# Performance work log

Hardware: AMD Instinct MI355X
Metric: run time of the kernel (lower is better)

Reference implementation:

```python
import jax, jax.numpy as jnp
import numpy as np

SEGMENT_LENGTHS = [2048, 4096, 8192]
DILATION_RATES = [1, 2, 4]
RING_SIZE = 4


def _head_groups(h, g):
    base, rem = divmod(h, g)
    return [base + (1 if i < rem else 0) for i in range(g)]


def _dilation_pattern(n, seg, r, group_idx):
    # Per-segment dilated index pattern of total length n (index_select target).
    s = min(seg, n)
    off = group_idx % r
    base = (off + np.arange(0, s, r)) % s          # stride-r indices within segment
    pat_seg = np.tile(base, r)[:s]                  # repeat to fill segment length
    nseg = n // s
    pat = (pat_seg[None, :] + np.arange(nseg)[:, None] * s).reshape(-1)
    return pat


def _apply_dilation(x):
    # x: (b, n, h, d). Gather along sequence per head group.
    b, n, h, d = x.shape
    groups = _head_groups(h, len(SEGMENT_LENGTHS))
    outs, hs = [], 0
    for i, (seg, r, g) in enumerate(zip(SEGMENT_LENGTHS, DILATION_RATES, groups)):
        if g == 0:
            continue
        pat = jnp.asarray(_dilation_pattern(n, seg, r, i))
        outs.append(x[:, pat, hs:hs + g, :])
        hs += g
    return jnp.concatenate(outs, axis=2)


def setup_inputs() -> dict:
    key = jax.random.key(0)
    k1, k2, k3 = jax.random.split(key, 3)
    shape = (1, 8192, 16, 64)
    return {
        "q": jax.random.normal(k1, shape, dtype=jnp.float32),
        "k": jax.random.normal(k2, shape, dtype=jnp.float32),
        "v": jax.random.normal(k3, shape, dtype=jnp.float32),
    }


def reference(q, k, v):
    b, n, h, d = q.shape
    scale = 1.0 / jnp.sqrt(jnp.asarray(d, q.dtype))
    chunk = n // RING_SIZE

    # Dilate queries once; dilate each local KV chunk (ring-distributed layout).
    qt = _apply_dilation(q).transpose(0, 2, 1, 3)   # (b, h, n, d)

    acc_out = jnp.zeros((b, h, n, d), q.dtype)
    acc_lse = jnp.full((b, h, n), -jnp.inf, q.dtype)

    # Simulated ring pass: iterate over KV chunks with online-LSE accumulation.
    for c in range(RING_SIZE):
        kc = _apply_dilation(k[:, c * chunk:(c + 1) * chunk])  # (b, chunk, h, d)
        vc = _apply_dilation(v[:, c * chunk:(c + 1) * chunk])
        scores = jnp.einsum('bhqd,bkhd->bhqk', qt, kc) * scale
        lse_c = jax.nn.logsumexp(scores, axis=-1)              # (b, h, n)
        out_c = jnp.einsum('bhqk,bkhd->bhqd',
                           jax.nn.softmax(scores, axis=-1), vc)
        new_lse = jnp.logaddexp(acc_lse, lse_c)
        w_old = jnp.exp(acc_lse - new_lse)[..., None]
        w_new = jnp.exp(lse_c - new_lse)[..., None]
        acc_out = w_old * acc_out + w_new * out_c
        acc_lse = new_lse

    return acc_out.transpose(0, 2, 1, 3)  # (b, n, h, d)
```

## Files before the change

kernel.cpp:

```cpp
#include <hip/hip_runtime.h>
#include <hip/hip_bf16.h>
#include <math.h>

typedef __attribute__((ext_vector_type(4))) float f32x4;
typedef __attribute__((ext_vector_type(8))) short bf16x8;
typedef __attribute__((ext_vector_type(4))) short s16x4;

#define NH 16
#define HD 64
#define BM 128
#define BM2 256
#define BN 64
#define WM 32
#define LDS_K 72
#define TILE2_B 16384
#define WS_FB 0ull

#define OPART5_OFF 20447232ull
#define LPART5_OFF (OPART5_OFF + 25165824ull)
#define WS5_NEEDED (LPART5_OFF + 393216ull)

__device__ __forceinline__ short f2bf(float f) {
    union { float f; unsigned u; } x; x.f = f;
    unsigned r = x.u + 0x7fffu + ((x.u >> 16) & 1u);
    return (short)(r >> 16);
}
__device__ __forceinline__ unsigned pack2bf(float a, float b) {
    union { float f; unsigned u; } x, y; x.f = a; y.f = b;
    return __builtin_amdgcn_perm(y.u + 0x8000u, x.u + 0x8000u, 0x07060302u);
}
__device__ __forceinline__ float elem(const float4& r, int j) {
    return ((const float*)&r)[j];
}
__device__ __forceinline__ size_t head_base2(int h) {
    if (h < 6)  return (size_t)h * (128 * TILE2_B);
    if (h < 11) return 6ull * (128 * TILE2_B) + (size_t)(h - 6) * (64 * TILE2_B);
    return 6ull * (128 * TILE2_B) + 5ull * (64 * TILE2_B) + (size_t)(h - 11) * (32 * TILE2_B);
}

__global__ __launch_bounds__(256)
void rda_pack2(const float* __restrict__ K, const float* __restrict__ V, char* __restrict__ W) {
    int bid = blockIdx.x;
    int h, t, type;
    if (bid < 768)       { type = 0; h = bid >> 7;                t = bid & 127; }
    else if (bid < 1088) { type = 1; h = 6 + ((bid - 768) >> 6);  t = (bid - 768) & 63; }
    else                 { type = 2; h = 11 + ((bid - 1088) >> 5); t = (bid - 1088) & 31; }
    int rate = 1 << type, off = type;
    char* tile = W + head_base2(h) + (size_t)t * TILE2_B;
    int tid = threadIdx.x;
    {
        int row = tid >> 2, c = (tid & 3) * 16;
        int pos = rate * (t * 64 + row) + off;
        const float* p = K + ((size_t)pos * NH + h) * HD + c;
        float4 a0 = ((const float4*)p)[0], a1 = ((const float4*)p)[1];
        float4 a2 = ((const float4*)p)[2], a3 = ((const float4*)p)[3];
        uint4 d0, d1;
        d0.x = pack2bf(elem(a0,0), elem(a0,1)); d0.y = pack2bf(elem(a0,2), elem(a0,3));
        d0.z = pack2bf(elem(a1,0), elem(a1,1)); d0.w = pack2bf(elem(a1,2), elem(a1,3));
        d1.x = pack2bf(elem(a2,0), elem(a2,1)); d1.y = pack2bf(elem(a2,2), elem(a2,3));
        d1.z = pack2bf(elem(a3,0), elem(a3,1)); d1.w = pack2bf(elem(a3,2), elem(a3,3));
        int L = row * 128 + c * 2;
        int sw = (row & 7) << 4;
        *(uint4*)(tile + (L ^ sw)) = d0;
        *(uint4*)(tile + ((L + 16) ^ sw)) = d1;
    }
    {
        int vr = (tid & 15) * 4, vc = (tid >> 4) * 4;
        float4 vv[4];
#pragma unroll
        for (int i = 0; i < 4; ++i) {
            int pos = rate * (t * 64 + vr + i) + off;
            vv[i] = *(const float4*)(V + ((size_t)pos * NH + h) * HD + vc);
        }
#pragma unroll
        for (int j = 0; j < 4; ++j) {
            uint2 w;
            w.x = pack2bf(elem(vv[0], j), elem(vv[1], j));
            w.y = pack2bf(elem(vv[2], j), elem(vv[3], j));
            int rr = vc + j;
            int L = rr * 128 + vr * 2;
            *(uint2*)(tile + 8192 + (L ^ ((rr & 7) << 4))) = w;
        }
    }
}

__global__ __launch_bounds__(512, 4)
void rda_attn_w8s(const float* __restrict__ Q, char* __restrict__ W, float* __restrict__ O) {
    __shared__ __align__(16) short sKV[2 * 8192];
    __shared__ __align__(16) short sP[8][1024];

    int bid = blockIdx.x;
    int h, mb, type, kc, nst, sid;
    if (bid < 384)      { type = 0; h = bid >> 6; int rem = bid & 63; mb = rem >> 1; kc = rem & 1; nst = 64; sid = bid; }
    else if (bid < 464) { type = 1; int rel = bid - 384; h = 6 + (rel >> 4); mb = rel & 15; kc = 0; nst = 64; sid = -1; }
    else                { type = 2; int rel = bid - 464; h = 11 + (rel >> 3); mb = rel & 7; kc = 0; nst = 32; sid = -1; }
    int rate = 1 << type;
    int off  = type;
    int kb0  = kc * 64;

    int tid  = threadIdx.x;
    int wave = tid >> 6;
    int lane = tid & 63;
    int ln   = lane & 15;
    int quad = lane >> 4;

    const float SC = 0.125f * 1.4426950408889634f;

    int qbase = mb * BM2 + wave * WM;
    bf16x8 qf[2][2];
#pragma unroll
    for (int mt = 0; mt < 2; ++mt) {
        int u = qbase + mt * 16 + ln;
        size_t base = ((size_t)(rate * u + off) * NH + h) * HD;
#pragma unroll
        for (int ks = 0; ks < 2; ++ks) {
            const float* p = Q + base + ks * 32 + quad * 8;
            float4 a = ((const float4*)p)[0];
            float4 b = ((const float4*)p)[1];
            union { uint4 u4; bf16x8 f; } cv;
            cv.u4.x = pack2bf(elem(a,0)*SC, elem(a,1)*SC);
            cv.u4.y = pack2bf(elem(a,2)*SC, elem(a,3)*SC);
            cv.u4.z = pack2bf(elem(b,0)*SC, elem(b,1)*SC);
            cv.u4.w = pack2bf(elem(b,2)*SC, elem(b,3)*SC);
            qf[mt][ks] = cv.f;
        }
    }

    f32x4 acc[2][4];
#pragma unroll
    for (int mt = 0; mt < 2; ++mt)
#pragma unroll
        for (int dt = 0; dt < 4; ++dt) acc[mt][dt] = (f32x4){0.f, 0.f, 0.f, 0.f};
    float lp[2] = {0.f, 0.f};

    const char* gh = W + head_base2(h);

    auto stage = [&](const char* gt, int lB) {
#pragma unroll
        for (int r = 0; r < 2; ++r) {
            int c = r * 8192 + tid * 16;
            __builtin_amdgcn_global_load_lds(
                (const __attribute__((address_space(1))) unsigned*)(gt + c),
                (__attribute__((address_space(3))) unsigned*)((char*)sKV + lB + c),
                16, 0, 0);
        }
    };

    stage(gh + (size_t)kb0 * TILE2_B, 0);
    int pB = 0;

    char* pbase = (char*)&sP[wave][0];

    for (int i = 0; i < nst; ++i) {
        int kb = kb0 + i;
        __syncthreads();

        if (i + 1 < nst) stage(gh + (size_t)(kb + 1) * TILE2_B, pB ^ TILE2_B);

        const char* sKb = (const char*)sKV + pB;
        const char* sVb = sKb + 8192;

#pragma unroll
        for (int x = 0; x < 2; ++x) {
            f32x4 st[2][2];
            __builtin_amdgcn_s_setprio(1);
#pragma unroll
            for (int kk = 0; kk < 2; ++kk) {
                int ra = (2 * x + kk) * 16 + ln;
                int sw = (ra & 7) << 4;
                bf16x8 a0 = *(const bf16x8*)(sKb + ((ra * 128 + quad * 16) ^ sw));
                bf16x8 a1 = *(const bf16x8*)(sKb + ((ra * 128 + 64 + quad * 16) ^ sw));
#pragma unroll
                for (int mt = 0; mt < 2; ++mt) {
                    f32x4 c = (f32x4){0.f, 0.f, 0.f, 0.f};
                    c = __builtin_amdgcn_mfma_f32_16x16x32_bf16(a0, qf[mt][0], c, 0, 0, 0);
                    c = __builtin_amdgcn_mfma_f32_16x16x32_bf16(a1, qf[mt][1], c, 0, 0, 0);
                    st[kk][mt] = c;
                }
            }
            __builtin_amdgcn_s_setprio(0);

#pragma unroll
            for (int mt = 0; mt < 2; ++mt)
#pragma unroll
                for (int kk = 0; kk < 2; ++kk) {
                    float p0 = __builtin_amdgcn_exp2f(st[kk][mt][0]);
                    float p1 = __builtin_amdgcn_exp2f(st[kk][mt][1]);
                    float p2 = __builtin_amdgcn_exp2f(st[kk][mt][2]);
                    float p3 = __builtin_amdgcn_exp2f(st[kk][mt][3]);
                    lp[mt] += (p0 + p1) + (p2 + p3);
                    uint2 pk;
                    pk.x = pack2bf(p0, p1);
                    pk.y = pack2bf(p2, p3);
                    int prow = mt * 16 + ln;
                    int Lb = prow * 64 + kk * 32 + quad * 8;
                    *(uint2*)(pbase + (Lb ^ (((prow >> 1) & 3) << 4))) = pk;
                }
            __asm__ volatile("s_waitcnt lgkmcnt(0)" ::: "memory");

            __builtin_amdgcn_s_setprio(1);
            int b0 = (ln * 64 + quad * 16) ^ (((ln >> 1) & 3) << 4);
            int b1 = ((16 + ln) * 64 + quad * 16) ^ ((((16 + ln) >> 1) & 3) << 4);
            bf16x8 pa0 = *(bf16x8*)(pbase + b0);
            bf16x8 pa1 = *(bf16x8*)(pbase + b1);
#pragma unroll
            for (int dt = 0; dt < 4; ++dt) {
                int rv = dt * 16 + ln;
                bf16x8 vb = *(const bf16x8*)(sVb + ((rv * 128 + x * 64 + quad * 16) ^ ((rv & 7) << 4)));
                acc[0][dt] = __builtin_amdgcn_mfma_f32_16x16x32_bf16(pa0, vb, acc[0][dt], 0, 0, 0);
                acc[1][dt] = __builtin_amdgcn_mfma_f32_16x16x32_bf16(pa1, vb, acc[1][dt], 0, 0, 0);
            }
            __builtin_amdgcn_s_setprio(0);
        }
        pB ^= TILE2_B;
    }

#pragma unroll
    for (int mt = 0; mt < 2; ++mt) {
        lp[mt] += __shfl_xor(lp[mt], 16);
        lp[mt] += __shfl_xor(lp[mt], 32);
    }

    if (type == 0) {
        float* Op = (float*)(W + OPART5_OFF) + (size_t)sid * (BM2 * HD);
        float* Lp = (float*)(W + LPART5_OFF) + (size_t)sid * BM2;
#pragma unroll
        for (int mt = 0; mt < 2; ++mt) {
            if (quad == 0) Lp[wave * WM + mt * 16 + ln] = lp[mt];
#pragma unroll
            for (int r = 0; r < 4; ++r) {
                int ql = wave * WM + mt * 16 + quad * 4 + r;
#pragma unroll
                for (int dt = 0; dt < 4; ++dt)
                    Op[ql * HD + dt * 16 + ln] = acc[mt][dt][r];
            }
        }
    } else {
#pragma unroll
        for (int mt = 0; mt < 2; ++mt)
#pragma unroll
            for (int r = 0; r < 4; ++r) {
                float lO = __shfl(lp[mt], quad * 4 + r);
                float inv = 1.0f / lO;
                int u = qbase + mt * 16 + quad * 4 + r;
#pragma unroll
                for (int dt = 0; dt < 4; ++dt) {
                    float val = acc[mt][dt][r] * inv;
                    int dcol = dt * 16 + ln;
                    if (type == 1) {
                        int r0 = ((u >> 11) << 12) + (u & 2047);
                        O[((size_t)r0 * NH + h) * HD + dcol] = val;
                        O[((size_t)(r0 + 2048) * NH + h) * HD + dcol] = val;
                    } else {
#pragma unroll
                        for (int t = 0; t < 4; ++t)
                            O[((size_t)(u + t * 2048) * NH + h) * HD + dcol] = val;
                    }
                }
            }
    }
}

__global__ __launch_bounds__(256)
void rda_comb5(const char* __restrict__ W, float* __restrict__ O) {
    int c = blockIdx.x;
    int h = c >> 5, mb = c & 31;
    int s0 = c * 2;

    const float* P0 = (const float*)(W + OPART5_OFF) + (size_t)s0 * (BM2 * HD);
    const float* L0 = (const float*)(W + LPART5_OFF) + (size_t)s0 * BM2;

    __shared__ float sInv[BM2];
    int tid = threadIdx.x;
    sInv[tid] = 1.0f / (L0[tid] + L0[BM2 + tid]);
    __syncthreads();

#pragma unroll
    for (int i = 0; i < 16; ++i) {
        int f = i * 256 + tid;
        int q = f >> 4, d4 = f & 15;
        float4 a = ((const float4*)P0)[f];
        float4 b = ((const float4*)(P0 + BM2 * HD))[f];
        float inv = sInv[q];
        float4 v;
        v.x = (a.x + b.x) * inv; v.y = (a.y + b.y) * inv;
        v.z = (a.z + b.z) * inv; v.w = (a.w + b.w) * inv;
        int u = mb * BM2 + q;
        *(float4*)&O[((size_t)u * NH + h) * HD + d4 * 4] = v;
    }
}

__global__ __launch_bounds__(256, 2)
void rda_attn_fb(const float* __restrict__ Q, const float* __restrict__ K,
                 const float* __restrict__ V, float* __restrict__ O) {
    __shared__ short sK[BN * LDS_K];
    __shared__ short sVT[HD * LDS_K];
    __shared__ short sP[4][WM * LDS_K];

    int bid = blockIdx.x;
    int h, mb, type;
    if (bid < 384)      { type = 0; h = bid >> 6;               mb = bid & 63; }
    else if (bid < 544) { type = 1; h = 6 + ((bid - 384) >> 5); mb = (bid - 384) & 31; }
    else                { type = 2; h = 11 + ((bid - 544) >> 4); mb = (bid - 544) & 15; }
    int rate = 1 << type;
    int off  = type;
    int nsteps = 128 >> type;

    int tid  = threadIdx.x;
    int wave = tid >> 6;
    int lane = tid & 63;
    int ln   = lane & 15;
    int quad = lane >> 4;

    const float SC = 0.125f * 1.4426950408889634f;

    int qbase = mb * BM + wave * WM;
    bf16x8 qf[2][2];
#pragma unroll
    for (int mt = 0; mt < 2; ++mt) {
        int u = qbase + mt * 16 + ln;
        size_t base = ((size_t)(rate * u + off) * NH + h) * HD;
#pragma unroll
        for (int ks = 0; ks < 2; ++ks) {
            const float* p = Q + base + ks * 32 + quad * 8;
            float4 a = ((const float4*)p)[0];
            float4 b = ((const float4*)p)[1];
            bf16x8 f;
#pragma unroll
            for (int i = 0; i < 4; ++i) { f[i] = f2bf(elem(a, i) * SC); f[4 + i] = f2bf(elem(b, i) * SC); }
            qf[mt][ks] = f;
        }
    }

    f32x4 acc[2][4];
#pragma unroll
    for (int mt = 0; mt < 2; ++mt)
#pragma unroll
        for (int dt = 0; dt < 4; ++dt) acc[mt][dt] = (f32x4){0.f, 0.f, 0.f, 0.f};
    float m_i[2] = {-INFINITY, -INFINITY};
    float l_i[2] = {0.f, 0.f};

    int srow = tid >> 2, sc0 = (tid & 3) * 16;
    int vr = (tid >> 4) * 4, vc = (tid & 15) * 4;

    for (int kb = 0; kb < nsteps; ++kb) {
        {
            int kpos = rate * (kb * BN + srow) + off;
            const float* p = K + ((size_t)kpos * NH + h) * HD + sc0;
            float4 kv0 = ((const float4*)p)[0], kv1 = ((const float4*)p)[1];
            float4 kv2 = ((const float4*)p)[2], kv3 = ((const float4*)p)[3];
            bf16x8 f0, f1;
#pragma unroll
            for (int i = 0; i < 4; ++i) {
                f0[i] = f2bf(elem(kv0, i)); f0[4 + i] = f2bf(elem(kv1, i));
                f1[i] = f2bf(elem(kv2, i)); f1[4 + i] = f2bf(elem(kv3, i));
            }
            *(bf16x8*)&sK[srow * LDS_K + sc0] = f0;
            *(bf16x8*)&sK[srow * LDS_K + sc0 + 8] = f1;
        }
        {
            float4 vv[4];
#pragma unroll
            for (int i = 0; i < 4; ++i) {
                int kpos = rate * (kb * BN + vr + i) + off;
                vv[i] = *(const float4*)(V + ((size_t)kpos * NH + h) * HD + vc);
            }
#pragma unroll
            for (int j = 0; j < 4; ++j) {
                s16x4 t;
                t[0] = f2bf(elem(vv[0], j)); t[1] = f2bf(elem(vv[1], j));
                t[2] = f2bf(elem(vv[2], j)); t[3] = f2bf(elem(vv[3], j));
                *(s16x4*)&sVT[(vc + j) * LDS_K + vr] = t;
            }
        }
        __syncthreads();

        f32x4 st[4][2];
#pragma unroll
        for (int kt = 0; kt < 4; ++kt) {
            bf16x8 a0 = *(bf16x8*)&sK[(kt * 16 + ln) * LDS_K + quad * 8];
            bf16x8 a1 = *(bf16x8*)&sK[(kt * 16 + ln) * LDS_K + 32 + quad * 8];
#pragma unroll
            for (int mt = 0; mt < 2; ++mt) {
                f32x4 c = (f32x4){0.f, 0.f, 0.f, 0.f};
                c = __builtin_amdgcn_mfma_f32_16x16x32_bf16(a0, qf[mt][0], c, 0, 0, 0);
                c = __builtin_amdgcn_mfma_f32_16x16x32_bf16(a1, qf[mt][1], c, 0, 0, 0);
                st[kt][mt] = c;
            }
        }

#pragma unroll
        for (int mt = 0; mt < 2; ++mt) {
            float tmax = -INFINITY;
#pragma unroll
            for (int kt = 0; kt < 4; ++kt)
#pragma unroll
                for (int r = 0; r < 4; ++r) tmax = fmaxf(tmax, st[kt][mt][r]);
            tmax = fmaxf(tmax, __shfl_xor(tmax, 16));
            tmax = fmaxf(tmax, __shfl_xor(tmax, 32));
            float mnew = fmaxf(m_i[mt], tmax);
            float al = exp2f(m_i[mt] - mnew);
            m_i[mt] = mnew;
            float rs = 0.f;
#pragma unroll
            for (int kt = 0; kt < 4; ++kt)
#pragma unroll
                for (int r = 0; r < 4; ++r) {
                    float pe = exp2f(st[kt][mt][r] - mnew);
                    st[kt][mt][r] = pe;
                    rs += pe;
                }
            rs += __shfl_xor(rs, 16);
            rs += __shfl_xor(rs, 32);
            l_i[mt] = l_i[mt] * al + rs;
#pragma unroll
            for (int r = 0; r < 4; ++r) {
                float aO = __shfl(al, quad * 4 + r);
#pragma unroll
                for (int dt = 0; dt < 4; ++dt) acc[mt][dt][r] *= aO;
            }
        }

#pragma unroll
        for (int mt = 0; mt < 2; ++mt)
#pragma unroll
            for (int kt = 0; kt < 4; ++kt) {
                s16x4 pk;
                pk[0] = f2bf(st[kt][mt][0]); pk[1] = f2bf(st[kt][mt][1]);
                pk[2] = f2bf(st[kt][mt][2]); pk[3] = f2bf(st[kt][mt][3]);
                *(s16x4*)&sP[wave][(mt * 16 + ln) * LDS_K + kt * 16 + quad * 4] = pk;
            }
        __asm__ volatile("s_waitcnt lgkmcnt(0)" ::: "memory");

#pragma unroll
        for (int ksk = 0; ksk < 2; ++ksk) {
            bf16x8 pa0 = *(bf16x8*)&sP[wave][(ln) * LDS_K + ksk * 32 + quad * 8];
            bf16x8 pa1 = *(bf16x8*)&sP[wave][(16 + ln) * LDS_K + ksk * 32 + quad * 8];
#pragma unroll
            for (int dt = 0; dt < 4; ++dt) {
                bf16x8 vb = *(bf16x8*)&sVT[(dt * 16 + ln) * LDS_K + ksk * 32 + quad * 8];
                acc[0][dt] = __builtin_amdgcn_mfma_f32_16x16x32_bf16(pa0, vb, acc[0][dt], 0, 0, 0);
                acc[1][dt] = __builtin_amdgcn_mfma_f32_16x16x32_bf16(pa1, vb, acc[1][dt], 0, 0, 0);
            }
        }
        __syncthreads();
    }

#pragma unroll
    for (int mt = 0; mt < 2; ++mt) {
#pragma unroll
        for (int r = 0; r < 4; ++r) {
            float lO = __shfl(l_i[mt], quad * 4 + r);
            float inv = 1.0f / lO;
            int u = qbase + mt * 16 + quad * 4 + r;
#pragma unroll
            for (int dt = 0; dt < 4; ++dt) {
                float val = acc[mt][dt][r] * inv;
                int dcol = dt * 16 + ln;
                if (type == 0) {
                    O[((size_t)u * NH + h) * HD + dcol] = val;
                } else if (type == 1) {
                    int r0 = ((u >> 11) << 12) + (u & 2047);
                    O[((size_t)r0 * NH + h) * HD + dcol] = val;
                    O[((size_t)(r0 + 2048) * NH + h) * HD + dcol] = val;
                } else {
#pragma unroll
                    for (int t = 0; t < 4; ++t)
                        O[((size_t)(u + t * 2048) * NH + h) * HD + dcol] = val;
                }
            }
        }
    }
}

extern "C" void kernel_launch(void* const* d_in, const int* in_sizes, int n_in,
                              void* d_out, int out_size, void* d_ws, size_t ws_size,
                              hipStream_t stream) {
    (void)in_sizes; (void)n_in; (void)out_size;
    const float* q = (const float*)d_in[0];
    const float* k = (const float*)d_in[1];
    const float* v = (const float*)d_in[2];
    float* o = (float*)d_out;
    if (ws_size >= WS5_NEEDED && d_ws != nullptr) {
        rda_pack2<<<dim3(1248), dim3(256), 0, stream>>>(k, v, (char*)d_ws);
        rda_attn_w8s<<<dim3(504), dim3(512), 0, stream>>>(q, (char*)d_ws, o);
        rda_comb5<<<dim3(192), dim3(256), 0, stream>>>((const char*)d_ws, o);
    } else {
        rda_attn_fb<<<dim3(624), dim3(256), 0, stream>>>(q, k, v, o);
    }
}
```

Measured before the change: 293.0 us.

## Split KV further: 4-way for rate-1 heads, 2-way for rate-2 heads

The attention kernel now splits the key/value range into 32-tile chunks, so rate-1 heads use 4 partial blocks and rate-2 heads use 2 instead of one. The grid grows from 504 to 968 blocks. The combine kernel now sums 4 or 2 partials and, for rate-2 heads, writes each result to both duplicated rows. This is meant to improve load balance and occupancy across CUs, at the cost of more partial-output workspace traffic and a heavier combine pass.

```diff
diff --git a/kernel.cpp b/kernel.cpp
--- a/kernel.cpp
+++ b/kernel.cpp
@@ -14,11 +14,10 @@
 #define WM 32
 #define LDS_K 72
 #define TILE2_B 16384
-#define WS_FB 0ull
-
-#define OPART5_OFF 20447232ull
-#define LPART5_OFF (OPART5_OFF + 25165824ull)
-#define WS5_NEEDED (LPART5_OFF + 393216ull)
+
+#define OPART6_OFF 20447232ull
+#define LPART6_OFF (OPART6_OFF + 60817408ull)
+#define WS6_NEEDED (LPART6_OFF + 950272ull)
 
 __device__ __forceinline__ short f2bf(float f) {
     union { float f; unsigned u; } x; x.f = f;
@@ -90,13 +89,13 @@
     __shared__ __align__(16) short sP[8][1024];
 
     int bid = blockIdx.x;
-    int h, mb, type, kc, nst, sid;
-    if (bid < 384)      { type = 0; h = bid >> 6; int rem = bid & 63; mb = rem >> 1; kc = rem & 1; nst = 64; sid = bid; }
-    else if (bid < 464) { type = 1; int rel = bid - 384; h = 6 + (rel >> 4); mb = rel & 15; kc = 0; nst = 64; sid = -1; }
-    else                { type = 2; int rel = bid - 464; h = 11 + (rel >> 3); mb = rel & 7; kc = 0; nst = 32; sid = -1; }
+    int h, mb, type, kc, sid;
+    if (bid < 768)      { type = 0; h = bid >> 7; int rem = bid & 127; mb = rem >> 2; kc = rem & 3; sid = bid; }
+    else if (bid < 928) { type = 1; int rel = bid - 768; h = 6 + (rel >> 5); int rem = rel & 31; mb = rem >> 1; kc = rem & 1; sid = bid; }
+    else                { type = 2; int rel = bid - 928; h = 11 + (rel >> 3); mb = rel & 7; kc = 0; sid = -1; }
     int rate = 1 << type;
     int off  = type;
-    int kb0  = kc * 64;
+    int kb0  = kc * 32;
 
     int tid  = threadIdx.x;
     int wave = tid >> 6;
@@ -151,11 +150,11 @@
 
     char* pbase = (char*)&sP[wave][0];
 
-    for (int i = 0; i < nst; ++i) {
+    for (int i = 0; i < 32; ++i) {
         int kb = kb0 + i;
         __syncthreads();
 
-        if (i + 1 < nst) stage(gh + (size_t)(kb + 1) * TILE2_B, pB ^ TILE2_B);
+        if (i + 1 < 32) stage(gh + (size_t)(kb + 1) * TILE2_B, pB ^ TILE2_B);
 
         const char* sKb = (const char*)sKV + pB;
         const char* sVb = sKb + 8192;
@@ -221,21 +220,7 @@
         lp[mt] += __shfl_xor(lp[mt], 32);
     }
 
-    if (type == 0) {
-        float* Op = (float*)(W + OPART5_OFF) + (size_t)sid * (BM2 * HD);
-        float* Lp = (float*)(W + LPART5_OFF) + (size_t)sid * BM2;
-#pragma unroll
-        for (int mt = 0; mt < 2; ++mt) {
-            if (quad == 0) Lp[wave * WM + mt * 16 + ln] = lp[mt];
-#pragma unroll
-            for (int r = 0; r < 4; ++r) {
-                int ql = wave * WM + mt * 16 + quad * 4 + r;
-#pragma unroll
-                for (int dt = 0; dt < 4; ++dt)
-                    Op[ql * HD + dt * 16 + ln] = acc[mt][dt][r];
-            }
-        }
-    } else {
+    if (type == 2) {
 #pragma unroll
         for (int mt = 0; mt < 2; ++mt)
 #pragma unroll
@@ -247,32 +232,45 @@
                 for (int dt = 0; dt < 4; ++dt) {
                     float val = acc[mt][dt][r] * inv;
                     int dcol = dt * 16 + ln;
-                    if (type == 1) {
-                        int r0 = ((u >> 11) << 12) + (u & 2047);
-                        O[((size_t)r0 * NH + h) * HD + dcol] = val;
-                        O[((size_t)(r0 + 2048) * NH + h) * HD + dcol] = val;
-                    } else {
-#pragma unroll
-                        for (int t = 0; t < 4; ++t)
-                            O[((size_t)(u + t * 2048) * NH + h) * HD + dcol] = val;
-                    }
+#pragma unroll
+                    for (int t = 0; t < 4; ++t)
+                        O[((size_t)(u + t * 2048) * NH + h) * HD + dcol] = val;
                 }
             }
+    } else {
+        float* Op = (float*)(W + OPART6_OFF) + (size_t)sid * (BM2 * HD);
+        float* Lp = (float*)(W + LPART6_OFF) + (size_t)sid * BM2;
+#pragma unroll
+        for (int mt = 0; mt < 2; ++mt) {
+            if (quad == 0) Lp[wave * WM + mt * 16 + ln] = lp[mt];
+#pragma unroll
+            for (int r = 0; r < 4; ++r) {
+                int ql = wave * WM + mt * 16 + quad * 4 + r;
+#pragma unroll
+                for (int dt = 0; dt < 4; ++dt)
+                    Op[ql * HD + dt * 16 + ln] = acc[mt][dt][r];
+            }
+        }
     }
 }
 
 __global__ __launch_bounds__(256)
-void rda_comb5(const char* __restrict__ W, float* __restrict__ O) {
+void rda_comb6(const char* __restrict__ W, float* __restrict__ O) {
     int c = blockIdx.x;
-    int h = c >> 5, mb = c & 31;
-    int s0 = c * 2;
-
-    const float* P0 = (const float*)(W + OPART5_OFF) + (size_t)s0 * (BM2 * HD);
-    const float* L0 = (const float*)(W + LPART5_OFF) + (size_t)s0 * BM2;
+    int h, mb, type, s0, np;
+    if (c < 192) { type = 0; h = c >> 5;              mb = c & 31; s0 = (h * 32 + mb) * 4; np = 4; }
+    else         { type = 1; int rel = c - 192; h = 6 + (rel >> 4); mb = rel & 15; s0 = 768 + rel * 2; np = 2; }
+
+    const float* P0 = (const float*)(W + OPART6_OFF) + (size_t)s0 * (BM2 * HD);
+    const float* L0 = (const float*)(W + LPART6_OFF) + (size_t)s0 * BM2;
 
     __shared__ float sInv[BM2];
     int tid = threadIdx.x;
-    sInv[tid] = 1.0f / (L0[tid] + L0[BM2 + tid]);
+    {
+        float s = L0[tid] + L0[BM2 + tid];
+        if (np == 4) s += L0[2 * BM2 + tid] + L0[3 * BM2 + tid];
+        sInv[tid] = 1.0f / s;
+    }
     __syncthreads();
 
 #pragma unroll
@@ -281,12 +279,23 @@
         int q = f >> 4, d4 = f & 15;
         float4 a = ((const float4*)P0)[f];
         float4 b = ((const float4*)(P0 + BM2 * HD))[f];
+        float4 v;
+        v.x = a.x + b.x; v.y = a.y + b.y; v.z = a.z + b.z; v.w = a.w + b.w;
+        if (np == 4) {
+            float4 e = ((const float4*)(P0 + 2 * BM2 * HD))[f];
+            float4 g = ((const float4*)(P0 + 3 * BM2 * HD))[f];
+            v.x += e.x + g.x; v.y += e.y + g.y; v.z += e.z + g.z; v.w += e.w + g.w;
+        }
         float inv = sInv[q];
-        float4 v;
-        v.x = (a.x + b.x) * inv; v.y = (a.y + b.y) * inv;
-        v.z = (a.z + b.z) * inv; v.w = (a.w + b.w) * inv;
+        v.x *= inv; v.y *= inv; v.z *= inv; v.w *= inv;
         int u = mb * BM2 + q;
-        *(float4*)&O[((size_t)u * NH + h) * HD + d4 * 4] = v;
+        if (type == 0) {
+            *(float4*)&O[((size_t)u * NH + h) * HD + d4 * 4] = v;
+        } else {
+            int r0 = ((u >> 11) << 12) + (u & 2047);
+            *(float4*)&O[((size_t)r0 * NH + h) * HD + d4 * 4] = v;
+            *(float4*)&O[((size_t)(r0 + 2048) * NH + h) * HD + d4 * 4] = v;
+        }
     }
 }
 
@@ -481,10 +490,10 @@
     const float* k = (const float*)d_in[1];
     const float* v = (const float*)d_in[2];
     float* o = (float*)d_out;
-    if (ws_size >= WS5_NEEDED && d_ws != nullptr) {
+    if (ws_size >= WS6_NEEDED && d_ws != nullptr) {
         rda_pack2<<<dim3(1248), dim3(256), 0, stream>>>(k, v, (char*)d_ws);
-        rda_attn_w8s<<<dim3(504), dim3(512), 0, stream>>>(q, (char*)d_ws, o);
-        rda_comb5<<<dim3(192), dim3(256), 0, stream>>>((const char*)d_ws, o);
+        rda_attn_w8s<<<dim3(968), dim3(512), 0, stream>>>(q, (char*)d_ws, o);
+        rda_comb6<<<dim3(272), dim3(256), 0, stream>>>((const char*)d_ws, o);
     } else {
         rda_attn_fb<<<dim3(624), dim3(256), 0, stream>>>(q, k, v, o);
     }
```

Result: no change. 296.3 us (+1.1%).
